# Optimization experiments

Hardware: AMD Instinct MI355X
Metric: run time of the kernel (lower is better)

## Reference

```python
import jax, jax.numpy as jnp
import numpy as np

B, C, H, W = 32, 1024, 32, 32  # N = H*W must equal C for the attn_c * attn_s broadcast
C8 = C // 8


def setup_inputs() -> dict:
    key = jax.random.key(0)
    ks = jax.random.split(key, 9)
    s = 1.0 / np.sqrt(C)
    return {
        "z": jax.random.normal(ks[0], (B, C, H, W), jnp.float32),
        "x": jax.random.normal(ks[1], (B, C, H, W), jnp.float32),
        "y": jax.random.normal(ks[2], (B, C, H, W), jnp.float32),
        "Wq": jax.random.normal(ks[3], (C8, C), jnp.float32) * s,
        "bq": jax.random.normal(ks[4], (C8,), jnp.float32) * 0.01,
        "Wk": jax.random.normal(ks[5], (C8, C), jnp.float32) * s,
        "bk": jax.random.normal(ks[6], (C8,), jnp.float32) * 0.01,
        "Wv": jax.random.normal(ks[7], (C, C), jnp.float32) * s,
        "bv": jax.random.normal(ks[8], (C,), jnp.float32) * 0.01,
    }


def reference(z, x, y, Wq, bq, Wk, bk, Wv, bv):
    b, c, h, w = x.shape
    n = h * w
    xf = x.reshape(b, c, n)
    yf = y.reshape(b, c, n)
    zf = z.reshape(b, c, n)

    # 1x1 convs == channel matmuls
    q = jnp.einsum('oc,bcn->bon', Wq, xf) + bq[None, :, None]   # (B, C/8, N)
    k = jnp.einsum('oc,bcn->bon', Wk, yf) + bk[None, :, None]   # (B, C/8, N)

    # channel-projected spatial attention: (B, N, N)
    energy_c = jnp.einsum('bcn,bcm->bnm', q, k)
    attention_c = jax.nn.softmax(energy_c, axis=-1)

    # raw channel attention: (B, C, C)
    energy_s = jnp.einsum('bcn,bdn->bcd', xf, yf)
    energy_s = jnp.max(energy_s, axis=-1, keepdims=True) - energy_s
    attention_s = jax.nn.softmax(energy_s, axis=-1)

    # multiplicative combine + third softmax (requires N == C)
    attention = jax.nn.softmax(attention_c * attention_s, axis=-1)

    v = jnp.einsum('oc,bcn->bon', Wv, zf) + bv[None, :, None]   # (B, C, N)
    # out[b,c,m] = sum_n v[b,c,n] * attention[b,m,n]  (value @ attention^T)
    out = jnp.einsum('bcn,bmn->bcm', v, attention)
    return z + out.reshape(b, c, h, w)
```

## Files before the change

kernel.cpp:

```cpp
#include <hip/hip_runtime.h>
#include <hip/hip_bf16.h>

typedef __attribute__((ext_vector_type(8))) short s8_t;
typedef __attribute__((ext_vector_type(4))) float f4_t;

__device__ __forceinline__ unsigned short f2bf(float f) {
  union { float f; unsigned u; } x; x.f = f;
  unsigned r = x.u + 0x7fffu + ((x.u >> 16) & 1u);
  return (unsigned short)(r >> 16);
}

__device__ __forceinline__ void split1(float v, unsigned short& h, unsigned short& l) {
  unsigned b = __float_as_uint(v);
  unsigned hb = b & 0xFFFF0000u;
  h = (unsigned short)(b >> 16);
  float lo = v - __uint_as_float(hb);
  l = (unsigned short)(__float_as_uint(lo) >> 16);
}

__device__ __forceinline__ void split2(float e0, float e1, unsigned& hp, unsigned& lp) {
  unsigned b0 = __float_as_uint(e0), b1 = __float_as_uint(e1);
  unsigned h0 = b0 & 0xFFFF0000u, h1 = b1 & 0xFFFF0000u;
  hp = (b0 >> 16) | h1;
  float l0 = e0 - __uint_as_float(h0), l1 = e1 - __uint_as_float(h1);
  lp = (__float_as_uint(l0) >> 16) | (__float_as_uint(l1) & 0xFFFF0000u);
}

__device__ __forceinline__ void gload16(const void* g, void* l) {
  __builtin_amdgcn_global_load_lds(
      (const __attribute__((address_space(1))) void*)g,
      (__attribute__((address_space(3))) void*)l, 16, 0, 0);
}

__device__ __forceinline__ void swz_grid(int& bx, int& by, int& bz) {
  const int gx = gridDim.x, gy = gridDim.y;
  const int nwg = gx * gy * gridDim.z;
  const int flat = (blockIdx.z * gy + blockIdx.y) * gx + blockIdx.x;
  const int s = (flat & 7) * (nwg >> 3) + (flat >> 3);
  bx = s % gx;
  const int r = s / gx;
  by = r % gy;
  bz = r / gy;
}

__global__ __launch_bounds__(256) void k_convert(const float* __restrict__ in,
                                                 unsigned short* __restrict__ out, int n) {
  int i = (blockIdx.x * 256 + threadIdx.x) * 8;
  if (i >= n) return;
  float4 a = *(const float4*)(in + i);
  float4 b = *(const float4*)(in + i + 4);
  ushort4 u0; u0.x = f2bf(a.x); u0.y = f2bf(a.y); u0.z = f2bf(a.z); u0.w = f2bf(a.w);
  ushort4 u1; u1.x = f2bf(b.x); u1.y = f2bf(b.y); u1.z = f2bf(b.z); u1.w = f2bf(b.w);
  *(ushort4*)(out + i) = u0;
  *(ushort4*)(out + i + 4) = u1;
}

__global__ __launch_bounds__(256) void k_tsplitT(const float* __restrict__ in,
                                                 unsigned short* __restrict__ th,
                                                 unsigned short* __restrict__ tl) {
  __shared__ float tile[64][65];
  const int t = threadIdx.x, bz = blockIdx.z;
  const int r0 = blockIdx.y * 64, c0 = blockIdx.x * 64;
  const float* ip = in + (size_t)bz * 1048576;
  const size_t ob = (size_t)bz * 1048576;
  const int tr = t >> 4, tc = (t & 15) * 4;
#pragma unroll
  for (int p = 0; p < 4; ++p) {
    int r = p * 16 + tr;
    float4 v = *(const float4*)(ip + (size_t)(r0 + r) * 1024 + c0 + tc);
    tile[r][tc] = v.x; tile[r][tc + 1] = v.y; tile[r][tc + 2] = v.z; tile[r][tc + 3] = v.w;
  }
  __syncthreads();
#pragma unroll
  for (int p = 0; p < 4; ++p) {
    int n = p * 16 + tr;
    float a = tile[tc][n], b = tile[tc + 1][n], c = tile[tc + 2][n], d = tile[tc + 3][n];
    ushort4 h, l;
    split1(a, h.x, l.x); split1(b, h.y, l.y); split1(c, h.z, l.z); split1(d, h.w, l.w);
    *(ushort4*)(th + ob + (size_t)(c0 + n) * 1024 + r0 + tc) = h;
    *(ushort4*)(tl + ob + (size_t)(c0 + n) * 1024 + r0 + tc) = l;
  }
}

__global__ __launch_bounds__(256) void k_transpbf(const float* __restrict__ in,
                                                  unsigned short* __restrict__ outt) {
  __shared__ unsigned short tile[64][72];
  const int t = threadIdx.x, b = blockIdx.z;
  const int r0 = blockIdx.y * 64, c0 = blockIdx.x * 64;
  const float* ip = in + (size_t)b * 1048576;
  const int tr = t >> 4, tc = (t & 15) * 4;
#pragma unroll
  for (int p = 0; p < 4; ++p) {
    int r = p * 16 + tr;
    float4 v = *(const float4*)(ip + (size_t)(r0 + r) * 1024 + c0 + tc);
    tile[r][tc] = f2bf(v.x); tile[r][tc + 1] = f2bf(v.y);
    tile[r][tc + 2] = f2bf(v.z); tile[r][tc + 3] = f2bf(v.w);
  }
  __syncthreads();
#pragma unroll
  for (int p = 0; p < 4; ++p) {
    int n = p * 16 + tr;
    ushort4 w;
    w.x = tile[tc][n]; w.y = tile[tc + 1][n]; w.z = tile[tc + 2][n]; w.w = tile[tc + 3][n];
    *(ushort4*)(outt + (size_t)b * 1048576 + (size_t)(c0 + n) * 1024 + r0 + tc) = w;
  }
}

__device__ __forceinline__ void split_write_swz(unsigned short* buf, int w0, int w1,
                                                const float* av, const float* bv) {
  unsigned ah[8], al[8], bh[8], bl[8];
#pragma unroll
  for (int p = 0; p < 8; ++p) {
    split2(av[2 * p], av[2 * p + 1], ah[p], al[p]);
    split2(bv[2 * p], bv[2 * p + 1], bh[p], bl[p]);
  }
  *(uint4*)(buf + w0) = *(uint4*)(ah);
  *(uint4*)(buf + w1) = *(uint4*)(ah + 4);
  *(uint4*)(buf + 4096 + w0) = *(uint4*)(al);
  *(uint4*)(buf + 4096 + w1) = *(uint4*)(al + 4);
  *(uint4*)(buf + 8192 + w0) = *(uint4*)(bh);
  *(uint4*)(buf + 8192 + w1) = *(uint4*)(bh + 4);
  *(uint4*)(buf + 12288 + w0) = *(uint4*)(bl);
  *(uint4*)(buf + 12288 + w1) = *(uint4*)(bl + 4);
}

template <int BIAS_MODE>
__global__ __launch_bounds__(256) void k_mfma3(
    const float* __restrict__ A, int lda, long long sA,
    const float* __restrict__ B, int ldb, long long sB,
    float* __restrict__ C, int ldc, long long sC,
    const float* __restrict__ bias, int K) {
  __shared__ __align__(16) unsigned short sm[16384];
  int bxs, bys, bz; swz_grid(bxs, bys, bz);
  const int tid = threadIdx.x;
  const int lane = tid & 63, wave = tid >> 6;
  const int wr = wave >> 1, wc = wave & 1;
  const int m0 = bxs * 128, n0 = bys * 128;

  const int sr = tid >> 1, sh = (tid & 1) * 16;
  const float* ag = A + (long long)bz * sA + (long long)(m0 + sr) * lda + sh;
  const float* bg = B + (long long)bz * sB + (long long)(n0 + sr) * ldb + sh;
  const int swm = (sr >> 1) & 3;
  const int s0 = (tid & 1) * 2;
  const int w0 = sr * 32 + (s0 ^ swm) * 8;
  const int w1 = sr * 32 + ((s0 + 1) ^ swm) * 8;

  const int lr = lane & 15, lg = lane >> 4;
  const int rdm = (lr >> 1) & 3;
  const int fa = (wr * 64 + lr) * 32 + (lg ^ rdm) * 8;
  const int fb = (wc * 64 + lr) * 32 + (lg ^ rdm) * 8;

  f4_t acc[4][4];
#pragma unroll
  for (int i = 0; i < 4; ++i)
#pragma unroll
    for (int j = 0; j < 4; ++j) acc[i][j] = (f4_t)0.f;

  for (int k0 = 0; k0 < K; k0 += 32) {
    float av[16], bv[16];
#pragma unroll
    for (int p = 0; p < 4; ++p) {
      *(float4*)(av + p * 4) = *(const float4*)(ag + p * 4);
      *(float4*)(bv + p * 4) = *(const float4*)(bg + p * 4);
    }
    split_write_swz(sm, w0, w1, av, bv);
    ag += 32; bg += 32;
    __syncthreads();
    const unsigned short* Ahp = sm;
    const unsigned short* Alp = sm + 4096;
    const unsigned short* Bhp = sm + 8192;
    const unsigned short* Blp = sm + 12288;
    s8_t fah[4], fbh[4], ftmp[4];
#pragma unroll
    for (int f = 0; f < 4; ++f) {
      fah[f] = *(const s8_t*)(Ahp + fa + f * 512);
      fbh[f] = *(const s8_t*)(Bhp + fb + f * 512);
    }
#pragma unroll
    for (int i = 0; i < 4; ++i)
#pragma unroll
      for (int j = 0; j < 4; ++j)
        acc[i][j] = __builtin_amdgcn_mfma_f32_16x16x32_bf16(fah[i], fbh[j], acc[i][j], 0, 0, 0);
#pragma unroll
    for (int f = 0; f < 4; ++f) ftmp[f] = *(const s8_t*)(Blp + fb + f * 512);
#pragma unroll
    for (int i = 0; i < 4; ++i)
#pragma unroll
      for (int j = 0; j < 4; ++j)
        acc[i][j] = __builtin_amdgcn_mfma_f32_16x16x32_bf16(fah[i], ftmp[j], acc[i][j], 0, 0, 0);
#pragma unroll
    for (int f = 0; f < 4; ++f) ftmp[f] = *(const s8_t*)(Alp + fa + f * 512);
#pragma unroll
    for (int i = 0; i < 4; ++i)
#pragma unroll
      for (int j = 0; j < 4; ++j)
        acc[i][j] = __builtin_amdgcn_mfma_f32_16x16x32_bf16(ftmp[i], fbh[j], acc[i][j], 0, 0, 0);
    __syncthreads();
  }

#pragma unroll
  for (int i = 0; i < 4; ++i) {
    const int rbase = m0 + wr * 64 + i * 16 + lg * 4;
#pragma unroll
    for (int j = 0; j < 4; ++j) {
      const int col = n0 + wc * 64 + j * 16 + lr;
      float bc = (BIAS_MODE == 2) ? bias[col] : 0.f;
#pragma unroll
      for (int e = 0; e < 4; ++e) {
        float v = acc[i][j][e];
        if (BIAS_MODE == 2) v += bc;
        C[(long long)bz * sC + (long long)(rbase + e) * ldc + col] = v;
      }
    }
  }
}

__global__ __launch_bounds__(256) void k_qk3p(
    const unsigned short* __restrict__ Axh, const unsigned short* __restrict__ Axl,
    const unsigned short* __restrict__ Ayh, const unsigned short* __restrict__ Ayl,
    const float* __restrict__ Wqf, const float* __restrict__ Wkf,
    const float* __restrict__ bqf, const float* __restrict__ bkf,
    float* __restrict__ Qt, float* __restrict__ Kt) {
  __shared__ __align__(16) unsigned short smAh[8192], smAl[8192];
  __shared__ __align__(16) unsigned short smBh[4096], smBl[4096];
  int bx, by, bz; swz_grid(bx, by, bz);
  const unsigned short* Ah = by ? Ayh : Axh;
  const unsigned short* Al = by ? Ayl : Axl;
  const float* Bf = by ? Wkf : Wqf;
  const float* bias = by ? bkf : bqf;
  float* Of = by ? Kt : Qt;

  const int tid = threadIdx.x, lane = tid & 63, wave = tid >> 6;
  const int wr = wave >> 1, wc = wave & 1;
  const int m0 = bx * 128;

  const int ch0 = wave * 64 + lane, ch1 = ch0 + 256;
  const int r0 = ch0 >> 2, kc0 = (((ch0 & 3) ^ ((ch0 >> 3) & 3))) * 8;
  const int r1 = ch1 >> 2, kc1 = (((ch1 & 3) ^ ((ch1 >> 3) & 3))) * 8;
  const unsigned short* pah0 = Ah + (long long)bz * 1048576 + (long long)(m0 + r0) * 1024 + kc0;
  const unsigned short* pah1 = Ah + (long long)bz * 1048576 + (long long)(m0 + r1) * 1024 + kc1;
  const unsigned short* pal0 = Al + (long long)bz * 1048576 + (long long)(m0 + r0) * 1024 + kc0;
  const unsigned short* pal1 = Al + (long long)bz * 1048576 + (long long)(m0 + r1) * 1024 + kc1;

  const int sr = tid >> 1, sh = (tid & 1) * 16;
  const float* bg = Bf + (long long)sr * 1024 + sh;
  const int swm = (sr >> 1) & 3;
  const int sB0 = (tid & 1) * 2;
  const int w0 = sr * 32 + (sB0 ^ swm) * 8;
  const int w1 = sr * 32 + ((sB0 + 1) ^ swm) * 8;

  const int lr = lane & 15, lg = lane >> 4;
  const int rdm = (lr >> 1) & 3;
  const int fa = (wr * 64 + lr) * 32 + (lg ^ rdm) * 8;
  const int fb = (wc * 64 + lr) * 32 + (lg ^ rdm) * 8;

  f4_t acc[4][4];
#pragma unroll
  for (int i = 0; i < 4; ++i)
#pragma unroll
    for (int j = 0; j < 4; ++j) acc[i][j] = (f4_t)0.f;

  float bv[16];
  auto stageA = [&](int b) {
    char* dh = (char*)smAh + b * 8192 + wave * 1024;
    char* dl = (char*)smAl + b * 8192 + wave * 1024;
    gload16(pah0, dh); gload16(pah1, dh + 4096);
    gload16(pal0, dl); gload16(pal1, dl + 4096);
    pah0 += 32; pah1 += 32; pal0 += 32; pal1 += 32;
  };
  auto loadW = [&]() {
#pragma unroll
    for (int p = 0; p < 4; ++p) *(float4*)(bv + p * 4) = *(const float4*)(bg + p * 4);
    bg += 32;
  };
  auto writeW = [&]() {
    unsigned bh[8], bl[8];
#pragma unroll
    for (int p = 0; p < 8; ++p) split2(bv[2 * p], bv[2 * p + 1], bh[p], bl[p]);
    *(uint4*)(smBh + w0) = *(uint4*)(bh);
    *(uint4*)(smBh + w1) = *(uint4*)(bh + 4);
    *(uint4*)(smBl + w0) = *(uint4*)(bl);
    *(uint4*)(smBl + w1) = *(uint4*)(bl + 4);
  };

  stageA(0);
  loadW();
  writeW();
  asm volatile("s_waitcnt vmcnt(0)" ::: "memory");
  __builtin_amdgcn_sched_barrier(0);
  __builtin_amdgcn_s_barrier();
  __builtin_amdgcn_sched_barrier(0);

  for (int t = 0; t < 32; ++t) {
    const bool more = (t < 31);
    if (more) { stageA((t + 1) & 1); loadW(); }
    const unsigned short* Ahp = smAh + (t & 1) * 4096;
    const unsigned short* Alp = smAl + (t & 1) * 4096;
    s8_t fah[4], fbh[4], ft[4];
#pragma unroll
    for (int f = 0; f < 4; ++f) {
      fah[f] = *(const s8_t*)(Ahp + fa + f * 512);
      fbh[f] = *(const s8_t*)(smBh + fb + f * 512);
    }
#pragma unroll
    for (int i = 0; i < 4; ++i)
#pragma unroll
      for (int j = 0; j < 4; ++j)
        acc[i][j] = __builtin_amdgcn_mfma_f32_16x16x32_bf16(fah[i], fbh[j], acc[i][j], 0, 0, 0);
#pragma unroll
    for (int f = 0; f < 4; ++f) ft[f] = *(const s8_t*)(smBl + fb + f * 512);
#pragma unroll
    for (int i = 0; i < 4; ++i)
#pragma unroll
      for (int j = 0; j < 4; ++j)
        acc[i][j] = __builtin_amdgcn_mfma_f32_16x16x32_bf16(fah[i], ft[j], acc[i][j], 0, 0, 0);
#pragma unroll
    for (int f = 0; f < 4; ++f) ft[f] = *(const s8_t*)(Alp + fa + f * 512);
#pragma unroll
    for (int i = 0; i < 4; ++i)
#pragma unroll
      for (int j = 0; j < 4; ++j)
        acc[i][j] = __builtin_amdgcn_mfma_f32_16x16x32_bf16(ft[i], fbh[j], acc[i][j], 0, 0, 0);
    __builtin_amdgcn_sched_barrier(0);
    __builtin_amdgcn_s_barrier();
    __builtin_amdgcn_sched_barrier(0);
    if (more) {
      writeW();
      asm volatile("s_waitcnt vmcnt(0)" ::: "memory");
    }
    __builtin_amdgcn_sched_barrier(0);
    __builtin_amdgcn_s_barrier();
    __builtin_amdgcn_sched_barrier(0);
  }

#pragma unroll
  for (int i = 0; i < 4; ++i) {
    const int rbase = m0 + wr * 64 + i * 16 + lg * 4;
#pragma unroll
    for (int j = 0; j < 4; ++j) {
      const int col = wc * 64 + j * 16 + lr;
      const float bc = bias[col];
#pragma unroll
      for (int e = 0; e < 4; ++e)
        Of[(long long)bz * 131072 + (long long)(rbase + e) * 128 + col] = acc[i][j][e] + bc;
    }
  }
}

template <int BIAS_MODE, bool OUT_BF16, bool RESID>
__global__ __launch_bounds__(512, 4) void k_mfma256(
    const unsigned short* __restrict__ A, int lda, long long sA,
    const unsigned short* __restrict__ B, int ldb, long long sB,
    void* __restrict__ Cp, int ldc, long long sC,
    const float* __restrict__ bias,
    const float* __restrict__ resid, long long sR, int K) {
  __shared__ __align__(16) unsigned short As[24576];
  __shared__ __align__(16) unsigned short Bs[12288];
  int bxs, bys, bz; swz_grid(bxs, bys, bz);
  const int tid = threadIdx.x;
  const int lane = tid & 63, wave = tid >> 6;
  const int wr = wave >> 1, wc = wave & 1;
  const int m0 = bxs * 256, n0 = bys * 128;

  const int cA0 = tid, cA1 = tid + 512;
  const int ra0 = cA0 >> 2, sa0 = ((cA0 & 3) ^ ((cA0 >> 3) & 3)) * 8;
  const int ra1 = cA1 >> 2, sa1 = ((cA1 & 3) ^ ((cA1 >> 3) & 3)) * 8;
  const unsigned short* pa0 = A + (long long)bz * sA + (long long)(m0 + ra0) * lda + sa0;
  const unsigned short* pa1 = A + (long long)bz * sA + (long long)(m0 + ra1) * lda + sa1;
  const unsigned short* pb0 = B + (long long)bz * sB + (long long)(n0 + ra0) * ldb + sa0;

  const int lr = lane & 15, lg = lane >> 4;
  const int rdm = (lr >> 1) & 3;
  const int fa = (wr * 64 + lr) * 32 + (lg ^ rdm) * 8;
  const int fb = (wc * 64 + lr) * 32 + (lg ^ rdm) * 8;

  f4_t acc[4][4];
#pragma unroll
  for (int i = 0; i < 4; ++i)
#pragma unroll
    for (int j = 0; j < 4; ++j) acc[i][j] = (f4_t)0.f;

  unsigned short* a0 = As;        unsigned short* a1 = As + 8192;
  unsigned short* a2 = As + 16384;
  unsigned short* b0 = Bs;        unsigned short* b1 = Bs + 4096;
  unsigned short* b2 = Bs + 8192;

  auto gA0 = [&](unsigned short* la) { gload16(pa0, (char*)la + wave * 1024); pa0 += 32; };
  auto gA1 = [&](unsigned short* la) { gload16(pa1, (char*)la + 8192 + wave * 1024); pa1 += 32; };
  auto gB0 = [&](unsigned short* lb) { gload16(pb0, (char*)lb + wave * 1024); pb0 += 32; };

  const int nt = K >> 5;
  gA0(a0); gA1(a0); gB0(b0);
  gA0(a1); gA1(a1); gB0(b1);

  for (int t = 0; t < nt; ++t) {
    if (t < nt - 1) asm volatile("s_waitcnt vmcnt(3)" ::: "memory");
    else            asm volatile("s_waitcnt vmcnt(0)" ::: "memory");
    __builtin_amdgcn_sched_barrier(0);
    __builtin_amdgcn_s_barrier();
    __builtin_amdgcn_sched_barrier(0);
    const bool pf = (t + 2 < nt);
    const unsigned short* ap = a0;
    const unsigned short* bp = b0;
    s8_t af[4], bf[4];
    if (pf) gA0(a2);
#pragma unroll
    for (int j = 0; j < 4; ++j) bf[j] = *(const s8_t*)(bp + fb + j * 512);
    if (pf) gA1(a2);
#pragma unroll
    for (int i = 0; i < 4; ++i) af[i] = *(const s8_t*)(ap + fa + i * 512);
    if (pf) gB0(b2);
    __builtin_amdgcn_s_setprio(1);
#pragma unroll
    for (int i = 0; i < 4; ++i)
#pragma unroll
      for (int j = 0; j < 4; ++j)
        acc[i][j] = __builtin_amdgcn_mfma_f32_16x16x32_bf16(af[i], bf[j], acc[i][j], 0, 0, 0);
    __builtin_amdgcn_s_setprio(0);
    unsigned short* ta = a0; a0 = a1; a1 = a2; a2 = ta;
    unsigned short* tb = b0; b0 = b1; b1 = b2; b2 = tb;
  }

#pragma unroll
  for (int i = 0; i < 4; ++i) {
    const int rbase = m0 + wr * 64 + i * 16 + lg * 4;
#pragma unroll
    for (int j = 0; j < 4; ++j) {
      const int col = n0 + wc * 64 + j * 16 + lr;
#pragma unroll
      for (int e = 0; e < 4; ++e) {
        const int row = rbase + e;
        float v = acc[i][j][e];
        if (BIAS_MODE == 1) v += bias[row];
        const long long off = (long long)bz * sC + (long long)row * ldc + col;
        if (RESID) v += resid[(long long)bz * sR + (long long)row * ldc + col];
        if (OUT_BF16) ((unsigned short*)Cp)[off] = f2bf(v);
        else          ((float*)Cp)[off] = v;
      }
    }
  }
}

__device__ __forceinline__ float wred_max(float v) {
#pragma unroll
  for (int o = 1; o < 64; o <<= 1) v = fmaxf(v, __shfl_xor(v, o, 64));
  return v;
}
__device__ __forceinline__ float wred_sum(float v) {
#pragma unroll
  for (int o = 1; o < 64; o <<= 1) v += __shfl_xor(v, o, 64);
  return v;
}

__global__ __launch_bounds__(256) void k_combine(float* __restrict__ ec,
                                                 const float* __restrict__ es) {
  const int lane = threadIdx.x & 63, wid = threadIdx.x >> 6;
  const size_t row = (size_t)blockIdx.x * 4 + wid;
  float* cp = ec + row * 1024;
  const float* sp = es + row * 1024;
  float4 c[4], s[4];
#pragma unroll
  for (int p = 0; p < 4; ++p) {
    c[p] = ((const float4*)cp)[lane * 4 + p];
    s[p] = ((const float4*)sp)[lane * 4 + p];
  }
  float mx = -3.4e38f;
#pragma unroll
  for (int p = 0; p < 4; ++p)
    mx = fmaxf(mx, fmaxf(fmaxf(c[p].x, c[p].y), fmaxf(c[p].z, c[p].w)));
  mx = wred_max(mx);
  float e[16], lsum = 0.f;
#pragma unroll
  for (int p = 0; p < 4; ++p) {
    e[4 * p]     = __expf(c[p].x - mx);
    e[4 * p + 1] = __expf(c[p].y - mx);
    e[4 * p + 2] = __expf(c[p].z - mx);
    e[4 * p + 3] = __expf(c[p].w - mx);
    lsum += e[4 * p] + e[4 * p + 1] + e[4 * p + 2] + e[4 * p + 3];
  }
  const float sc = wred_sum(lsum);
  float mt = -3.4e38f;
#pragma unroll
  for (int p = 0; p < 4; ++p)
    mt = fmaxf(mt, fmaxf(fmaxf(-s[p].x, -s[p].y), fmaxf(-s[p].z, -s[p].w)));
  mt = wred_max(mt);
  float f[16]; lsum = 0.f;
#pragma unroll
  for (int p = 0; p < 4; ++p) {
    f[4 * p]     = __expf(-s[p].x - mt);
    f[4 * p + 1] = __expf(-s[p].y - mt);
    f[4 * p + 2] = __expf(-s[p].z - mt);
    f[4 * p + 3] = __expf(-s[p].w - mt);
    lsum += f[4 * p] + f[4 * p + 1] + f[4 * p + 2] + f[4 * p + 3];
  }
  const float ss = wred_sum(lsum);
  const float rc = 1.f / sc, rs = 1.f / ss;
  float g[16]; lsum = 0.f;
#pragma unroll
  for (int q = 0; q < 16; ++q) {
    g[q] = __expf((e[q] * rc) * (f[q] * rs));
    lsum += g[q];
  }
  const float s3 = wred_sum(lsum);
  const float r3 = 1.f / s3;
#pragma unroll
  for (int p = 0; p < 4; ++p) {
    ushort4 o;
    o.x = f2bf(g[4 * p] * r3);     o.y = f2bf(g[4 * p + 1] * r3);
    o.z = f2bf(g[4 * p + 2] * r3); o.w = f2bf(g[4 * p + 3] * r3);
    ((ushort4*)cp)[lane * 4 + p] = o;
  }
}

extern "C" void kernel_launch(void* const* d_in, const int* in_sizes, int n_in,
                              void* d_out, int out_size, void* d_ws, size_t ws_size,
                              hipStream_t stream) {
  const float* z = (const float*)d_in[0];
  const float* x = (const float*)d_in[1];
  const float* y = (const float*)d_in[2];
  const float* Wq = (const float*)d_in[3];
  const float* bq = (const float*)d_in[4];
  const float* Wk = (const float*)d_in[5];
  const float* bk = (const float*)d_in[6];
  const float* Wv = (const float*)d_in[7];
  const float* bv = (const float*)d_in[8];
  float* out = (float*)d_out;

  char* ws = (char*)d_ws;
  unsigned short* yth = (unsigned short*)ws;
  unsigned short* ytl = yth + 33554432;
  float* es = (float*)ws;
  unsigned short* z_t = (unsigned short*)ws;
  unsigned short* v_bf = z_t + 33554432;
  char* wsB = ws + 134217728;
  unsigned short* xth = (unsigned short*)wsB;
  unsigned short* xtl = xth + 33554432;
  float* ec = (float*)wsB;
  unsigned short* attn = (unsigned short*)wsB;
  char* wsC = ws + 268435456;
  float* q_t = (float*)wsC;
  float* k_t = q_t + 4194304;
  unsigned short* wv = (unsigned short*)wsC;

  dim3 blk(256);
  hipLaunchKernelGGL(k_tsplitT, dim3(16, 16, 32), blk, 0, stream, x, xth, xtl);
  hipLaunchKernelGGL(k_tsplitT, dim3(16, 16, 32), blk, 0, stream, y, yth, ytl);
  hipLaunchKernelGGL(k_qk3p, dim3(8, 2, 32), blk, 0, stream,
                     xth, xtl, yth, ytl, Wq, Wk, bq, bk, q_t, k_t);
  hipLaunchKernelGGL((k_mfma3<0>), dim3(8, 8, 32), blk, 0, stream,
                     x, 1024, 1048576LL, y, 1024, 1048576LL, es, 1024, 1048576LL,
                     (const float*)nullptr, 1024);
  hipLaunchKernelGGL((k_mfma3<0>), dim3(8, 8, 32), blk, 0, stream,
                     q_t, 128, 131072LL, k_t, 128, 131072LL, ec, 1024, 1048576LL,
                     (const float*)nullptr, 128);
  hipLaunchKernelGGL(k_combine, dim3(8192), blk, 0, stream, ec, es);
  hipLaunchKernelGGL(k_transpbf, dim3(16, 16, 32), blk, 0, stream, z, z_t);
  hipLaunchKernelGGL(k_convert, dim3(512), blk, 0, stream, Wv, wv, 1048576);
  hipLaunchKernelGGL((k_mfma256<1, true, false>), dim3(4, 8, 32), dim3(512), 0, stream,
                     wv, 1024, 0LL, z_t, 1024, 1048576LL, (void*)v_bf, 1024, 1048576LL,
                     bv, (const float*)nullptr, 0LL, 1024);
  hipLaunchKernelGGL((k_mfma256<0, false, true>), dim3(4, 8, 32), dim3(512), 0, stream,
                     v_bf, 1024, 1048576LL, attn, 2048, 2097152LL, (void*)out, 1024, 1048576LL,
                     (const float*)nullptr, z, 1048576LL, 1024);
}
```

Before: 746.7 us.

## Replace split-bf16 GEMM with double-buffered async fp32 LDS staging kernel

The 3-pass split-bf16 GEMM used for the x·yᵀ and q·kᵀ energies is replaced. Fp32 tiles are now copied straight from global memory into XOR-swizzled LDS with global_load_lds, double-buffered so the next tile loads while the current one computes. The hi/lo bf16 split moves from the store side to the fragment-read side. This removes register staging and one barrier per k-step, and lets loads overlap the MFMA work. In exchange, LDS use doubles to 64 KB, each wave now splits redundantly in registers, and s_setprio hints are added.

```diff
diff --git a/kernel.cpp b/kernel.cpp
--- a/kernel.cpp
+++ b/kernel.cpp
@@ -24,6 +24,16 @@
   hp = (b0 >> 16) | h1;
   float l0 = e0 - __uint_as_float(h0), l1 = e1 - __uint_as_float(h1);
   lp = (__float_as_uint(l0) >> 16) | (__float_as_uint(l1) & 0xFFFF0000u);
+}
+
+__device__ __forceinline__ void split8(float4 u0, float4 u1, s8_t& hi, s8_t& lo) {
+  unsigned short h[8], l[8];
+  split1(u0.x, h[0], l[0]); split1(u0.y, h[1], l[1]);
+  split1(u0.z, h[2], l[2]); split1(u0.w, h[3], l[3]);
+  split1(u1.x, h[4], l[4]); split1(u1.y, h[5], l[5]);
+  split1(u1.z, h[6], l[6]); split1(u1.w, h[7], l[7]);
+#pragma unroll
+  for (int i = 0; i < 8; ++i) { hi[i] = (short)h[i]; lo[i] = (short)l[i]; }
 }
 
 __device__ __forceinline__ void gload16(const void* g, void* l) {
@@ -106,49 +116,32 @@
   }
 }
 
-__device__ __forceinline__ void split_write_swz(unsigned short* buf, int w0, int w1,
-                                                const float* av, const float* bv) {
-  unsigned ah[8], al[8], bh[8], bl[8];
-#pragma unroll
-  for (int p = 0; p < 8; ++p) {
-    split2(av[2 * p], av[2 * p + 1], ah[p], al[p]);
-    split2(bv[2 * p], bv[2 * p + 1], bh[p], bl[p]);
-  }
-  *(uint4*)(buf + w0) = *(uint4*)(ah);
-  *(uint4*)(buf + w1) = *(uint4*)(ah + 4);
-  *(uint4*)(buf + 4096 + w0) = *(uint4*)(al);
-  *(uint4*)(buf + 4096 + w1) = *(uint4*)(al + 4);
-  *(uint4*)(buf + 8192 + w0) = *(uint4*)(bh);
-  *(uint4*)(buf + 8192 + w1) = *(uint4*)(bh + 4);
-  *(uint4*)(buf + 12288 + w0) = *(uint4*)(bl);
-  *(uint4*)(buf + 12288 + w1) = *(uint4*)(bl + 4);
-}
-
-template <int BIAS_MODE>
-__global__ __launch_bounds__(256) void k_mfma3(
+__global__ __launch_bounds__(256, 2) void k_g3t(
     const float* __restrict__ A, int lda, long long sA,
     const float* __restrict__ B, int ldb, long long sB,
-    float* __restrict__ C, int ldc, long long sC,
-    const float* __restrict__ bias, int K) {
-  __shared__ __align__(16) unsigned short sm[16384];
+    float* __restrict__ C, int ldc, long long sC, int K) {
+  __shared__ __align__(16) float As[8192];
+  __shared__ __align__(16) float Bs[8192];
   int bxs, bys, bz; swz_grid(bxs, bys, bz);
   const int tid = threadIdx.x;
   const int lane = tid & 63, wave = tid >> 6;
   const int wr = wave >> 1, wc = wave & 1;
   const int m0 = bxs * 128, n0 = bys * 128;
 
-  const int sr = tid >> 1, sh = (tid & 1) * 16;
-  const float* ag = A + (long long)bz * sA + (long long)(m0 + sr) * lda + sh;
-  const float* bg = B + (long long)bz * sB + (long long)(n0 + sr) * ldb + sh;
-  const int swm = (sr >> 1) & 3;
-  const int s0 = (tid & 1) * 2;
-  const int w0 = sr * 32 + (s0 ^ swm) * 8;
-  const int w1 = sr * 32 + ((s0 + 1) ^ swm) * 8;
+  const float* pa[4];
+  const float* pb[4];
+#pragma unroll
+  for (int s = 0; s < 4; ++s) {
+    const int row = s * 32 + (tid >> 3);
+    const int gr = (tid & 7) ^ (row & 7);
+    pa[s] = A + (long long)bz * sA + (long long)(m0 + row) * lda + gr * 4;
+    pb[s] = B + (long long)bz * sB + (long long)(n0 + row) * ldb + gr * 4;
+  }
 
   const int lr = lane & 15, lg = lane >> 4;
-  const int rdm = (lr >> 1) & 3;
-  const int fa = (wr * 64 + lr) * 32 + (lg ^ rdm) * 8;
-  const int fb = (wc * 64 + lr) * 32 + (lg ^ rdm) * 8;
+  const int x7 = lr & 7;
+  const int g0 = (2 * lg) ^ x7;
+  const int g1 = (2 * lg + 1) ^ x7;
 
   f4_t acc[4][4];
 #pragma unroll
@@ -156,46 +149,75 @@
 #pragma unroll
     for (int j = 0; j < 4; ++j) acc[i][j] = (f4_t)0.f;
 
-  for (int k0 = 0; k0 < K; k0 += 32) {
-    float av[16], bv[16];
-#pragma unroll
-    for (int p = 0; p < 4; ++p) {
-      *(float4*)(av + p * 4) = *(const float4*)(ag + p * 4);
-      *(float4*)(bv + p * 4) = *(const float4*)(bg + p * 4);
-    }
-    split_write_swz(sm, w0, w1, av, bv);
-    ag += 32; bg += 32;
-    __syncthreads();
-    const unsigned short* Ahp = sm;
-    const unsigned short* Alp = sm + 4096;
-    const unsigned short* Bhp = sm + 8192;
-    const unsigned short* Blp = sm + 12288;
-    s8_t fah[4], fbh[4], ftmp[4];
+  float* cA = As;       float* cB = Bs;
+  float* nA = As + 4096; float* nB = Bs + 4096;
+
+  auto stageA = [&](float* buf) {
+#pragma unroll
+    for (int s = 0; s < 4; ++s) {
+      gload16(pa[s], (char*)buf + s * 4096 + wave * 1024);
+      pa[s] += 32;
+    }
+  };
+  auto stageB = [&](float* buf) {
+#pragma unroll
+    for (int s = 0; s < 4; ++s) {
+      gload16(pb[s], (char*)buf + s * 4096 + wave * 1024);
+      pb[s] += 32;
+    }
+  };
+
+  const int nt = K >> 5;
+  stageA(cA); stageB(cB);
+  asm volatile("s_waitcnt vmcnt(0)" ::: "memory");
+  __builtin_amdgcn_sched_barrier(0);
+  __builtin_amdgcn_s_barrier();
+  __builtin_amdgcn_sched_barrier(0);
+
+  for (int t = 0; t < nt; ++t) {
+    const bool pf = (t + 1 < nt);
+    if (pf) stageA(nA);
+    s8_t fah[4], fal[4], fbh[4], fbl[4];
 #pragma unroll
     for (int f = 0; f < 4; ++f) {
-      fah[f] = *(const s8_t*)(Ahp + fa + f * 512);
-      fbh[f] = *(const s8_t*)(Bhp + fb + f * 512);
-    }
+      const float* ar = cA + (wr * 64 + f * 16 + lr) * 32;
+      float4 u0 = *(const float4*)(ar + g0 * 4);
+      float4 u1 = *(const float4*)(ar + g1 * 4);
+      split8(u0, u1, fah[f], fal[f]);
+    }
+    if (pf) stageB(nB);
+#pragma unroll
+    for (int f = 0; f < 4; ++f) {
+      const float* br = cB + (wc * 64 + f * 16 + lr) * 32;
+      float4 u0 = *(const float4*)(br + g0 * 4);
+      float4 u1 = *(const float4*)(br + g1 * 4);
+      split8(u0, u1, fbh[f], fbl[f]);
+    }
+    __builtin_amdgcn_s_setprio(1);
 #pragma unroll
     for (int i = 0; i < 4; ++i)
 #pragma unroll
       for (int j = 0; j < 4; ++j)
         acc[i][j] = __builtin_amdgcn_mfma_f32_16x16x32_bf16(fah[i], fbh[j], acc[i][j], 0, 0, 0);
 #pragma unroll
-    for (int f = 0; f < 4; ++f) ftmp[f] = *(const s8_t*)(Blp + fb + f * 512);
-#pragma unroll
-    for (int i = 0; i < 4; ++i)
-#pragma unroll
-      for (int j = 0; j < 4; ++j)
-        acc[i][j] = __builtin_amdgcn_mfma_f32_16x16x32_bf16(fah[i], ftmp[j], acc[i][j], 0, 0, 0);
-#pragma unroll
-    for (int f = 0; f < 4; ++f) ftmp[f] = *(const s8_t*)(Alp + fa + f * 512);
-#pragma unroll
-    for (int i = 0; i < 4; ++i)
-#pragma unroll
-      for (int j = 0; j < 4; ++j)
-        acc[i][j] = __builtin_amdgcn_mfma_f32_16x16x32_bf16(ftmp[i], fbh[j], acc[i][j], 0, 0, 0);
-    __syncthreads();
+    for (int i = 0; i < 4; ++i)
+#pragma unroll
+      for (int j = 0; j < 4; ++j)
+        acc[i][j] = __builtin_amdgcn_mfma_f32_16x16x32_bf16(fah[i], fbl[j], acc[i][j], 0, 0, 0);
+#pragma unroll
+    for (int i = 0; i < 4; ++i)
+#pragma unroll
+      for (int j = 0; j < 4; ++j)
+        acc[i][j] = __builtin_amdgcn_mfma_f32_16x16x32_bf16(fal[i], fbh[j], acc[i][j], 0, 0, 0);
+    __builtin_amdgcn_s_setprio(0);
+    if (pf) {
+      asm volatile("s_waitcnt vmcnt(0)" ::: "memory");
+      __builtin_amdgcn_sched_barrier(0);
+      __builtin_amdgcn_s_barrier();
+      __builtin_amdgcn_sched_barrier(0);
+    }
+    float* tA = cA; cA = nA; nA = tA;
+    float* tB = cB; cB = nB; nB = tB;
   }
 
 #pragma unroll
@@ -204,13 +226,9 @@
 #pragma unroll
     for (int j = 0; j < 4; ++j) {
       const int col = n0 + wc * 64 + j * 16 + lr;
-      float bc = (BIAS_MODE == 2) ? bias[col] : 0.f;
-#pragma unroll
-      for (int e = 0; e < 4; ++e) {
-        float v = acc[i][j][e];
-        if (BIAS_MODE == 2) v += bc;
-        C[(long long)bz * sC + (long long)(rbase + e) * ldc + col] = v;
-      }
+#pragma unroll
+      for (int e = 0; e < 4; ++e)
+        C[(long long)bz * sC + (long long)(rbase + e) * ldc + col] = acc[i][j][e];
     }
   }
 }
@@ -547,12 +565,10 @@
   hipLaunchKernelGGL(k_tsplitT, dim3(16, 16, 32), blk, 0, stream, y, yth, ytl);
   hipLaunchKernelGGL(k_qk3p, dim3(8, 2, 32), blk, 0, stream,
                      xth, xtl, yth, ytl, Wq, Wk, bq, bk, q_t, k_t);
-  hipLaunchKernelGGL((k_mfma3<0>), dim3(8, 8, 32), blk, 0, stream,
-                     x, 1024, 1048576LL, y, 1024, 1048576LL, es, 1024, 1048576LL,
-                     (const float*)nullptr, 1024);
-  hipLaunchKernelGGL((k_mfma3<0>), dim3(8, 8, 32), blk, 0, stream,
-                     q_t, 128, 131072LL, k_t, 128, 131072LL, ec, 1024, 1048576LL,
-                     (const float*)nullptr, 128);
+  hipLaunchKernelGGL(k_g3t, dim3(8, 8, 32), blk, 0, stream,
+                     x, 1024, 1048576LL, y, 1024, 1048576LL, es, 1024, 1048576LL, 1024);
+  hipLaunchKernelGGL(k_g3t, dim3(8, 8, 32), blk, 0, stream,
+                     q_t, 128, 131072LL, k_t, 128, 131072LL, ec, 1024, 1048576LL, 128);
   hipLaunchKernelGGL(k_combine, dim3(8192), blk, 0, stream, ec, es);
   hipLaunchKernelGGL(k_transpbf, dim3(16, 16, 32), blk, 0, stream, z, z_t);
   hipLaunchKernelGGL(k_convert, dim3(512), blk, 0, stream, Wv, wv, 1048576);
```

Result: slower. 822.4 us (+10.1%).

## Double-buffer LDS in the split-bf16 MFMA GEMM with register prefetch

Applied to the files above, without the earlier changes.

The GEMM loop now keeps two shared-memory stages. Global loads for the next K-tile go into registers while MFMAs run on the current tile, and the split hi/lo values are written into the other buffer, so there is one barrier per iteration instead of two. It also raises wave priority around MFMA bursts with s_setprio and asks for two blocks per CU in the launch bounds. The cost is double the LDS footprint and more register pressure, and the raw s_barrier relies on the compiler inserting the LDS waitcnt.

```diff
diff --git a/kernel.cpp b/kernel.cpp
--- a/kernel.cpp
+++ b/kernel.cpp
@@ -125,12 +125,12 @@
 }
 
 template <int BIAS_MODE>
-__global__ __launch_bounds__(256) void k_mfma3(
+__global__ __launch_bounds__(256, 2) void k_mfma3(
     const float* __restrict__ A, int lda, long long sA,
     const float* __restrict__ B, int ldb, long long sB,
     float* __restrict__ C, int ldc, long long sC,
     const float* __restrict__ bias, int K) {
-  __shared__ __align__(16) unsigned short sm[16384];
+  __shared__ __align__(16) unsigned short sm[32768];
   int bxs, bys, bz; swz_grid(bxs, bys, bz);
   const int tid = threadIdx.x;
   const int lane = tid & 63, wave = tid >> 6;
@@ -156,46 +156,72 @@
 #pragma unroll
     for (int j = 0; j < 4; ++j) acc[i][j] = (f4_t)0.f;
 
-  for (int k0 = 0; k0 < K; k0 += 32) {
-    float av[16], bv[16];
-#pragma unroll
-    for (int p = 0; p < 4; ++p) {
-      *(float4*)(av + p * 4) = *(const float4*)(ag + p * 4);
-      *(float4*)(bv + p * 4) = *(const float4*)(bg + p * 4);
-    }
-    split_write_swz(sm, w0, w1, av, bv);
-    ag += 32; bg += 32;
-    __syncthreads();
-    const unsigned short* Ahp = sm;
-    const unsigned short* Alp = sm + 4096;
-    const unsigned short* Bhp = sm + 8192;
-    const unsigned short* Blp = sm + 12288;
+  const int nt = K >> 5;
+  float av[16], bv[16];
+  unsigned short* cur = sm;
+  unsigned short* nxt = sm + 16384;
+
+#pragma unroll
+  for (int p = 0; p < 4; ++p) {
+    *(float4*)(av + p * 4) = *(const float4*)(ag + p * 4);
+    *(float4*)(bv + p * 4) = *(const float4*)(bg + p * 4);
+  }
+  ag += 32; bg += 32;
+  split_write_swz(cur, w0, w1, av, bv);
+  __builtin_amdgcn_sched_barrier(0);
+  __builtin_amdgcn_s_barrier();
+  __builtin_amdgcn_sched_barrier(0);
+
+  for (int t = 0; t < nt; ++t) {
+    const bool more = (t + 1 < nt);
+    if (more) {
+#pragma unroll
+      for (int p = 0; p < 4; ++p) {
+        *(float4*)(av + p * 4) = *(const float4*)(ag + p * 4);
+        *(float4*)(bv + p * 4) = *(const float4*)(bg + p * 4);
+      }
+      ag += 32; bg += 32;
+    }
+    const unsigned short* Ahp = cur;
+    const unsigned short* Alp = cur + 4096;
+    const unsigned short* Bhp = cur + 8192;
+    const unsigned short* Blp = cur + 12288;
     s8_t fah[4], fbh[4], ftmp[4];
 #pragma unroll
     for (int f = 0; f < 4; ++f) {
       fah[f] = *(const s8_t*)(Ahp + fa + f * 512);
       fbh[f] = *(const s8_t*)(Bhp + fb + f * 512);
     }
+    __builtin_amdgcn_s_setprio(1);
 #pragma unroll
     for (int i = 0; i < 4; ++i)
 #pragma unroll
       for (int j = 0; j < 4; ++j)
         acc[i][j] = __builtin_amdgcn_mfma_f32_16x16x32_bf16(fah[i], fbh[j], acc[i][j], 0, 0, 0);
+    __builtin_amdgcn_s_setprio(0);
 #pragma unroll
     for (int f = 0; f < 4; ++f) ftmp[f] = *(const s8_t*)(Blp + fb + f * 512);
+    __builtin_amdgcn_s_setprio(1);
 #pragma unroll
     for (int i = 0; i < 4; ++i)
 #pragma unroll
       for (int j = 0; j < 4; ++j)
         acc[i][j] = __builtin_amdgcn_mfma_f32_16x16x32_bf16(fah[i], ftmp[j], acc[i][j], 0, 0, 0);
+    __builtin_amdgcn_s_setprio(0);
 #pragma unroll
     for (int f = 0; f < 4; ++f) ftmp[f] = *(const s8_t*)(Alp + fa + f * 512);
+    __builtin_amdgcn_s_setprio(1);
 #pragma unroll
     for (int i = 0; i < 4; ++i)
 #pragma unroll
       for (int j = 0; j < 4; ++j)
         acc[i][j] = __builtin_amdgcn_mfma_f32_16x16x32_bf16(ftmp[i], fbh[j], acc[i][j], 0, 0, 0);
-    __syncthreads();
+    __builtin_amdgcn_s_setprio(0);
+    if (more) split_write_swz(nxt, w0, w1, av, bv);
+    __builtin_amdgcn_sched_barrier(0);
+    __builtin_amdgcn_s_barrier();
+    __builtin_amdgcn_sched_barrier(0);
+    unsigned short* tmp = cur; cur = nxt; nxt = tmp;
   }
 
 #pragma unroll
```

Result: slower. 815.0 us (+9.1%).
